# Optimization experiments

Measured on AMD Instinct MI355X. Metric: run time of the kernel, lower is better.

## Reference

```python
import jax, jax.numpy as jnp
import numpy as np

EPS = 1e-5

def batchnorm2d(x, gamma, beta):
    # training-mode BN over (N, T, V) per channel; x: [N, C, T, V]
    mean = jnp.mean(x, axis=(0, 2, 3), keepdims=True)
    var = jnp.var(x, axis=(0, 2, 3), keepdims=True)
    xhat = (x - mean) * jax.lax.rsqrt(var + EPS)
    return xhat * gamma[None, :, None, None] + beta[None, :, None, None]

def temporal_shift(x, theta, stride):
    # learnable per-channel temporal shift with linear interpolation, zero pad
    # x: [N, C, T, V], theta: [C]
    N, C, T, V = x.shape
    T_out = T // stride
    t = jnp.arange(T_out, dtype=theta.dtype)
    pos = t[None, :] * stride + theta[:, None]          # [C, T_out]
    i0 = jnp.floor(pos).astype(jnp.int32)
    frac = (pos - i0.astype(theta.dtype))[None, :, :, None]  # [1,C,T_out,1]
    cidx = jnp.arange(C)[:, None]                        # [C, 1]

    def gather(idx):
        valid = (idx >= 0) & (idx < T)
        g = x[:, cidx, jnp.clip(idx, 0, T - 1), :]       # [N, C, T_out, V]
        return jnp.where(valid[None, :, :, None], g, 0.0)

    return gather(i0) * (1.0 - frac) + gather(i0 + 1) * frac

def setup_inputs() -> dict:
    key = jax.random.key(0)
    k = jax.random.split(key, 6)
    N, Cin, Cout, T, V = 64, 256, 256, 64, 25
    x = jax.random.normal(k[0], (N, Cin, T, V), dtype=jnp.float32)
    # kaiming normal fan_out for 1x1 conv: std = sqrt(2 / (Cout*1*1))
    conv_w = jax.random.normal(k[1], (Cout, Cin), dtype=jnp.float32) * np.float32(np.sqrt(2.0 / Cout))
    conv_b = jnp.zeros((Cout,), dtype=jnp.float32)
    bn1_g = jnp.ones((Cin,), dtype=jnp.float32)
    bn1_b = jnp.zeros((Cin,), dtype=jnp.float32)
    bn2_g = jnp.ones((Cin,), dtype=jnp.float32)   # bn_init(bn2, 1)
    bn2_b = jnp.zeros((Cin,), dtype=jnp.float32)
    theta_in = jax.random.uniform(k[2], (Cin,), jnp.float32, -1.0, 1.0)
    theta_out = jax.random.uniform(k[3], (Cout,), jnp.float32, -1.0, 1.0)
    return {"x": x, "conv_w": conv_w, "conv_b": conv_b,
            "bn1_g": bn1_g, "bn1_b": bn1_b, "bn2_g": bn2_g, "bn2_b": bn2_b,
            "theta_in": theta_in, "theta_out": theta_out}

def reference(x, conv_w, conv_b, bn1_g, bn1_b, bn2_g, bn2_b, theta_in, theta_out):
    stride = 1
    h = batchnorm2d(x, bn1_g, bn1_b)
    h = temporal_shift(h, theta_in, 1)
    h = jnp.einsum('nctv,oc->notv', h, conv_w) + conv_b[None, :, None, None]
    h = jax.nn.relu(h)
    h = temporal_shift(h, theta_out, stride)
    h = batchnorm2d(h, bn2_g, bn2_b)
    return h
```

## Files before the change

### kernel.cpp

```cpp
#include <hip/hip_runtime.h>


#define EPSV 1e-5f
constexpr int Nn = 64, Cc = 256, Tt = 64, Vv = 25;
constexpr int TV = Tt * Vv;
constexpr int CTV = Cc * TV;
constexpr float Minv = 1.0f / (Nn * TV);

typedef short short8 __attribute__((ext_vector_type(8)));
typedef float floatx4 __attribute__((ext_vector_type(4)));

__device__ __forceinline__ unsigned short f2bf(float f) {
    unsigned int u = __builtin_bit_cast(unsigned int, f);
    u += 0x7FFFu + ((u >> 16) & 1u);
    return (unsigned short)(u >> 16);
}
__device__ __forceinline__ float bf2f(unsigned short h) {
    unsigned int u = ((unsigned int)h) << 16;
    return __builtin_bit_cast(float, u);
}
__device__ __forceinline__ void gload_lds16(const void* g, void* l) {
    __builtin_amdgcn_global_load_lds((const __attribute__((address_space(1))) void*)g,
                                     (__attribute__((address_space(3))) void*)l, 16, 0, 0);
}

__global__ __launch_bounds__(256) void k_stats_shift(const float* __restrict__ x,
                                                     const float* __restrict__ theta,
                                                     float* __restrict__ sacc,
                                                     float* __restrict__ qacc,
                                                     unsigned short* __restrict__ ht) {
    int c0 = blockIdx.x * 64;
    int E0 = blockIdx.y * 200;
    int n  = blockIdx.z;
    int tid = threadIdx.x;
    __shared__ __attribute__((aligned(16))) float xt[256][68];
    __shared__ int   pd[64];
    __shared__ float pf[64];
    if (tid < 64) {
        float th = theta[c0 + tid];
        float fd = floorf(th);
        pd[tid] = (int)fd;
        pf[tid] = th - fd;
    }
    int lo = E0 - 28; if (lo < 0) lo = 0;
    int hi = E0 + 228; if (hi > 1600) hi = 1600;
    int ldsoff = lo - (E0 - 28);
    int nf4 = (hi - lo) >> 2;
    {
        int ci = tid >> 2, li = tid & 3;
        const float4* xrow = (const float4*)(x + (size_t)n * CTV + (size_t)(c0 + ci) * TV + lo);
        for (int i = li; i < nf4; i += 4) {
            float4 v = xrow[i];
            int r = ldsoff + i * 4;
            xt[r][ci] = v.x; xt[r + 1][ci] = v.y; xt[r + 2][ci] = v.z; xt[r + 3][ci] = v.w;
        }
    }
    __syncthreads();
    {
        int ci = tid >> 2, li = tid & 3;
        float s = 0.f, q = 0.f;
        for (int r = 28 + li; r < 228; r += 4) {
            float v = xt[r][ci];
            s += v; q += v * v;
        }
        s += __shfl_down(s, 2); q += __shfl_down(q, 2);
        s += __shfl_down(s, 1); q += __shfl_down(q, 1);
        if (li == 0) { atomicAdd(&sacc[c0 + ci], s); atomicAdd(&qacc[c0 + ci], q); }
    }
    int cseg = tid & 7, er = tid >> 3;
    int cb = cseg * 8;
    for (int it = 0; it < 7; ++it) {
        int tv_l = er + it * 32;
        if (tv_l >= 200) break;
        int e = E0 + tv_l;
        int t = e / 25;
        const float* rA = &xt[tv_l + 3][cb];
        const float* rB = &xt[tv_l + 28][cb];
        const float* rC = &xt[tv_l + 53][cb];
        float4 a0 = *(const float4*)rA, a1 = *(const float4*)(rA + 4);
        float4 b0 = *(const float4*)rB, b1 = *(const float4*)(rB + 4);
        float4 g0 = *(const float4*)rC, g1 = *(const float4*)(rC + 4);
        float A8[8] = {a0.x, a0.y, a0.z, a0.w, a1.x, a1.y, a1.z, a1.w};
        float B8[8] = {b0.x, b0.y, b0.z, b0.w, b1.x, b1.y, b1.z, b1.w};
        float C8[8] = {g0.x, g0.y, g0.z, g0.w, g1.x, g1.y, g1.z, g1.w};
        unsigned int w4[4];
#pragma unroll
        for (int k = 0; k < 8; ++k) {
            int c = cb + k;
            int d = pd[c]; float f = pf[c];
            int i0 = t + d;
            float x0 = (d < 0) ? A8[k] : B8[k];
            float x1 = (d < 0) ? B8[k] : C8[k];
            float v0 = ((unsigned)i0 < 64u) ? x0 : 0.f;
            float v1 = ((unsigned)(i0 + 1) < 64u) ? x1 : 0.f;
            unsigned short hb = f2bf(v0 + f * (v1 - v0));
            if (k & 1) w4[k >> 1] |= ((unsigned int)hb) << 16;
            else       w4[k >> 1] = hb;
        }
        uint4 st = { w4[0], w4[1], w4[2], w4[3] };
        *(uint4*)(ht + (size_t)(n * 1600 + e) * 256 + c0 + cb) = st;
    }
}

__global__ __launch_bounds__(256) void k_params(const float* __restrict__ w,
                                                const float* __restrict__ bias,
                                                const float* __restrict__ sacc,
                                                const float* __restrict__ qacc,
                                                const float* __restrict__ g,
                                                const float* __restrict__ b,
                                                const float* __restrict__ theta,
                                                unsigned short* __restrict__ wb,
                                                float* __restrict__ b2all,
                                                float* __restrict__ s0v,
                                                float* __restrict__ s63v) {
    int o = blockIdx.x, c = threadIdx.x;
    float mean = sacc[c] * Minv;
    float var  = qacc[c] * Minv - mean * mean;
    float sc = g[c] * rsqrtf(var + EPSV);
    float tc = b[c] - mean * sc;
    float th = theta[c];
    float fd = floorf(th);
    int d = (int)fd;
    float f = th - fd;
    float wv = w[o * 256 + c];
    wb[o * 256 + c] = f2bf(wv * sc);
    float wtc = wv * tc;
    float r0  = (d < 0) ? wtc * (1.f - f) : 0.f;
    float r63 = (d == 0) ? wtc * f : 0.f;
    for (int off = 32; off; off >>= 1) {
        wtc += __shfl_down(wtc, off);
        r0  += __shfl_down(r0, off);
        r63 += __shfl_down(r63, off);
    }
    __shared__ float aux[3][4];
    if ((c & 63) == 0) { int wv_i = c >> 6; aux[0][wv_i] = wtc; aux[1][wv_i] = r0; aux[2][wv_i] = r63; }
    __syncthreads();
    if (c == 0) {
        float sw  = aux[0][0] + aux[0][1] + aux[0][2] + aux[0][3];
        float s0  = aux[1][0] + aux[1][1] + aux[1][2] + aux[1][3];
        float s63 = aux[2][0] + aux[2][1] + aux[2][2] + aux[2][3];
        b2all[o] = bias[o] + sw;
        s0v[o] = s0;
        s63v[o] = s63;
    }
}

__global__ __launch_bounds__(256, 2) void k_gemm(const unsigned short* __restrict__ ht,
                                                 const unsigned short* __restrict__ wb,
                                                 const float* __restrict__ b2all,
                                                 const float* __restrict__ s0v,
                                                 const float* __restrict__ s63v,
                                                 unsigned short* __restrict__ y) {
    int j0 = blockIdx.x * 128;
    int tid = threadIdx.x;
    int w = tid >> 6, lane = tid & 63;
    int quad = lane >> 4, l16 = lane & 15;
    __shared__ __attribute__((aligned(16))) unsigned short smem[256 * 136];
    unsigned short* A = smem;
    unsigned short* B = smem + 256 * 32;
    floatx4 acc[4][8] = {};
    int srowA = w * 64 + (lane >> 2);
    int srowB = w * 32 + (lane >> 2);
    int skc = (lane & 3) * 8;
    const unsigned short* wp = wb + (size_t)srowA * 256 + skc;
    const unsigned short* hp = ht + (size_t)(j0 + srowB) * 256 + skc;
    for (int k0 = 0; k0 < 256; k0 += 32) {
        __syncthreads();
#pragma unroll
        for (int a = 0; a < 4; ++a)
            gload_lds16(wp + (size_t)a * 16 * 256 + k0, A + (w * 64 + a * 16) * 32);
#pragma unroll
        for (int a = 0; a < 2; ++a)
            gload_lds16(hp + (size_t)a * 16 * 256 + k0, B + (w * 32 + a * 16) * 32);
        __syncthreads();
        short8 af[4], bf[8];
#pragma unroll
        for (int m = 0; m < 4; ++m)
            af[m] = *(const short8*)&A[(w * 64 + m * 16 + l16) * 32 + quad * 8];
#pragma unroll
        for (int jt = 0; jt < 8; ++jt)
            bf[jt] = *(const short8*)&B[(jt * 16 + l16) * 32 + quad * 8];
#pragma unroll
        for (int m = 0; m < 4; ++m)
#pragma unroll
            for (int jt = 0; jt < 8; ++jt)
                acc[m][jt] = __builtin_amdgcn_mfma_f32_16x16x32_bf16(af[m], bf[jt], acc[m][jt], 0, 0, 0);
    }
    __syncthreads();
    unsigned short* Cl = smem;
#pragma unroll
    for (int m = 0; m < 4; ++m) {
        int ob = w * 64 + m * 16 + quad * 4;
#pragma unroll
        for (int r = 0; r < 4; ++r) {
            int o = ob + r;
            float bb = b2all[o], e0 = s0v[o], e63 = s63v[o];
#pragma unroll
            for (int jt = 0; jt < 8; ++jt) {
                int jj = j0 + jt * 16;
                int nn = jj / 1600;
                int tvb = jj - nn * 1600 + l16;
                float bia = bb - (tvb < 25 ? e0 : 0.f) - (tvb >= 1575 ? e63 : 0.f);
                float v = acc[m][jt][r] + bia;
                v = v > 0.f ? v : 0.f;
                Cl[o * 136 + jt * 16 + l16] = f2bf(v);
            }
        }
    }
    __syncthreads();
    int li = tid & 15, orow = tid >> 4;
#pragma unroll
    for (int pass = 0; pass < 16; ++pass) {
        int o = orow + pass * 16;
        uint4 vv = *(const uint4*)&Cl[o * 136 + li * 8];
        int j = j0 + li * 8;
        int nn = j / 1600;
        int tv = j - nn * 1600;
        *(uint4*)(y + (size_t)nn * CTV + (size_t)o * TV + tv) = vv;
    }
}

__global__ __launch_bounds__(256) void k_bn2_stats(const unsigned short* __restrict__ y,
                                                   const float* __restrict__ theta,
                                                   float* __restrict__ sacc,
                                                   float* __restrict__ qacc) {
    int o = blockIdx.y, ng = blockIdx.x, tid = threadIdx.x;
    __shared__ __attribute__((aligned(16))) unsigned short row[1600];
    float th = theta[o];
    float fd = floorf(th);
    int d = (int)fd;
    float f = th - fd;
    float s = 0.f, q = 0.f;
    for (int n = ng * 8; n < ng * 8 + 8; ++n) {
        const uint4* yp = (const uint4*)(y + (size_t)n * CTV + (size_t)o * TV);
        __syncthreads();
        if (tid < 200) ((uint4*)row)[tid] = yp[tid];
        __syncthreads();
        for (int e = tid; e < 1600; e += 256) {
            int t = e / 25, v = e - t * 25;
            int i0 = t + d, i1 = i0 + 1;
            float a0 = ((unsigned)i0 < 64u) ? bf2f(row[i0 * 25 + v]) : 0.f;
            float a1 = ((unsigned)i1 < 64u) ? bf2f(row[i1 * 25 + v]) : 0.f;
            float z = (1.f - f) * a0 + f * a1;
            s += z; q += z * z;
        }
    }
    for (int off = 32; off; off >>= 1) { s += __shfl_down(s, off); q += __shfl_down(q, off); }
    if ((tid & 63) == 0) { atomicAdd(&sacc[o], s); atomicAdd(&qacc[o], q); }
}

__global__ __launch_bounds__(256) void k_bn2_apply(const unsigned short* __restrict__ y,
                                                   const float* __restrict__ theta,
                                                   const float* __restrict__ sacc,
                                                   const float* __restrict__ qacc,
                                                   const float* __restrict__ g,
                                                   const float* __restrict__ b,
                                                   float* __restrict__ out) {
    int o = blockIdx.y, n = blockIdx.x, tid = threadIdx.x;
    __shared__ __attribute__((aligned(16))) unsigned short row[1600];
    float th = theta[o];
    float fd = floorf(th);
    int d = (int)fd;
    float f = th - fd;
    float mean = sacc[o] * Minv;
    float var = qacc[o] * Minv - mean * mean;
    float sc = g[o] * rsqrtf(var + EPSV);
    float tc = b[o] - mean * sc;
    const uint4* yp = (const uint4*)(y + (size_t)n * CTV + (size_t)o * TV);
    if (tid < 200) ((uint4*)row)[tid] = yp[tid];
    __syncthreads();
    float4* op = (float4*)(out + (size_t)n * CTV + (size_t)o * TV);
    for (int i = tid; i < 400; i += 256) {
        float4 r;
        int e = i * 4;
#pragma unroll
        for (int k = 0; k < 4; ++k) {
            int ee = e + k;
            int t = ee / 25, v = ee - t * 25;
            int i0 = t + d, i1 = i0 + 1;
            float a0 = ((unsigned)i0 < 64u) ? bf2f(row[i0 * 25 + v]) : 0.f;
            float a1 = ((unsigned)i1 < 64u) ? bf2f(row[i1 * 25 + v]) : 0.f;
            ((float*)&r)[k] = ((1.f - f) * a0 + f * a1) * sc + tc;
        }
        op[i] = r;
    }
}

extern "C" void kernel_launch(void* const* d_in, const int* in_sizes, int n_in,
                              void* d_out, int out_size, void* d_ws, size_t ws_size,
                              hipStream_t stream) {
    const float* x      = (const float*)d_in[0];
    const float* conv_w = (const float*)d_in[1];
    const float* conv_b = (const float*)d_in[2];
    const float* bn1_g  = (const float*)d_in[3];
    const float* bn1_b  = (const float*)d_in[4];
    const float* bn2_g  = (const float*)d_in[5];
    const float* bn2_b  = (const float*)d_in[6];
    const float* th_in  = (const float*)d_in[7];
    const float* th_out = (const float*)d_in[8];
    float* out = (float*)d_out;

    char* ws = (char*)d_ws;
    unsigned short* ht = (unsigned short*)ws;
    unsigned short* yy = (unsigned short*)(ws + 52428800);
    unsigned short* wb = (unsigned short*)(ws + 104857600);
    float* sacc1 = (float*)(ws + 104988672);
    float* qacc1 = sacc1 + 256;
    float* sacc2 = qacc1 + 256;
    float* qacc2 = sacc2 + 256;
    float* b2all = qacc2 + 256;
    float* s0v   = b2all + 256;
    float* s63v  = s0v + 256;

    hipMemsetAsync((void*)sacc1, 0, 4 * 256 * sizeof(float), stream);
    hipLaunchKernelGGL(k_stats_shift, dim3(4, 8, 64), dim3(256), 0, stream,
                       x, th_in, sacc1, qacc1, ht);
    hipLaunchKernelGGL(k_params, dim3(256), dim3(256), 0, stream,
                       conv_w, conv_b, sacc1, qacc1, bn1_g, bn1_b, th_in,
                       wb, b2all, s0v, s63v);
    hipLaunchKernelGGL(k_gemm, dim3(800), dim3(256), 0, stream,
                       ht, wb, b2all, s0v, s63v, yy);
    hipLaunchKernelGGL(k_bn2_stats, dim3(8, 256), dim3(256), 0, stream, yy, th_out, sacc2, qacc2);
    hipLaunchKernelGGL(k_bn2_apply, dim3(64, 256), dim3(256), 0, stream,
                       yy, th_out, sacc2, qacc2, bn2_g, bn2_b, out);
}
```

Measured before the change: 315.7 us.

## Derive BN2 stats algebraically from raw moments; bf16 LDS staging in shift kernel

```diff
diff --git a/kernel.cpp b/kernel.cpp
--- a/kernel.cpp
+++ b/kernel.cpp
@@ -18,6 +18,16 @@
 __device__ __forceinline__ float bf2f(unsigned short h) {
     unsigned int u = ((unsigned int)h) << 16;
     return __builtin_bit_cast(float, u);
+}
+__device__ __forceinline__ float bflo(unsigned int w) {
+    return __builtin_bit_cast(float, w << 16);
+}
+__device__ __forceinline__ float bfhi(unsigned int w) {
+    return __builtin_bit_cast(float, w & 0xFFFF0000u);
+}
+__device__ __forceinline__ void unp8v(uint4 u, float* o) {
+    o[0] = bflo(u.x); o[1] = bfhi(u.x); o[2] = bflo(u.y); o[3] = bfhi(u.y);
+    o[4] = bflo(u.z); o[5] = bfhi(u.z); o[6] = bflo(u.w); o[7] = bfhi(u.w);
 }
 __device__ __forceinline__ void gload_lds16(const void* g, void* l) {
     __builtin_amdgcn_global_load_lds((const __attribute__((address_space(1))) void*)g,
@@ -33,7 +43,7 @@
     int E0 = blockIdx.y * 200;
     int n  = blockIdx.z;
     int tid = threadIdx.x;
-    __shared__ __attribute__((aligned(16))) float xt[256][68];
+    __shared__ __attribute__((aligned(16))) unsigned short xt[256][68];
     __shared__ int   pd[64];
     __shared__ float pf[64];
     if (tid < 64) {
@@ -47,52 +57,67 @@
     int ldsoff = lo - (E0 - 28);
     int nf4 = (hi - lo) >> 2;
     {
-        int ci = tid >> 2, li = tid & 3;
-        const float4* xrow = (const float4*)(x + (size_t)n * CTV + (size_t)(c0 + ci) * TV + lo);
-        for (int i = li; i < nf4; i += 4) {
-            float4 v = xrow[i];
+        int cp = tid >> 3, li = tid & 7;
+        int ca = 2 * cp;
+        const float4* xr0 = (const float4*)(x + (size_t)n * CTV + (size_t)(c0 + ca) * TV + lo);
+        const float4* xr1 = (const float4*)(x + (size_t)n * CTV + (size_t)(c0 + ca + 1) * TV + lo);
+        float s0 = 0.f, q0 = 0.f, s1 = 0.f, q1 = 0.f;
+        for (int i = li; i < nf4; i += 8) {
+            float4 v0 = xr0[i], v1 = xr1[i];
             int r = ldsoff + i * 4;
-            xt[r][ci] = v.x; xt[r + 1][ci] = v.y; xt[r + 2][ci] = v.z; xt[r + 3][ci] = v.w;
+#pragma unroll
+            for (int k = 0; k < 4; ++k) {
+                float a = ((const float*)&v0)[k];
+                float b = ((const float*)&v1)[k];
+                bool in = (unsigned)(r + k - 28) < 200u;
+                if (in) { s0 += a; q0 += a * a; s1 += b; q1 += b * b; }
+                unsigned int pk = (unsigned int)f2bf(a) | (((unsigned int)f2bf(b)) << 16);
+                *(unsigned int*)&xt[r + k][ca] = pk;
+            }
+        }
+        for (int off = 4; off; off >>= 1) {
+            s0 += __shfl_down(s0, off); q0 += __shfl_down(q0, off);
+            s1 += __shfl_down(s1, off); q1 += __shfl_down(q1, off);
+        }
+        if (li == 0) {
+            atomicAdd(&sacc[c0 + ca], s0);     atomicAdd(&qacc[c0 + ca], q0);
+            atomicAdd(&sacc[c0 + ca + 1], s1); atomicAdd(&qacc[c0 + ca + 1], q1);
         }
     }
     __syncthreads();
-    {
-        int ci = tid >> 2, li = tid & 3;
-        float s = 0.f, q = 0.f;
-        for (int r = 28 + li; r < 228; r += 4) {
-            float v = xt[r][ci];
-            s += v; q += v * v;
-        }
-        s += __shfl_down(s, 2); q += __shfl_down(q, 2);
-        s += __shfl_down(s, 1); q += __shfl_down(q, 1);
-        if (li == 0) { atomicAdd(&sacc[c0 + ci], s); atomicAdd(&qacc[c0 + ci], q); }
-    }
     int cseg = tid & 7, er = tid >> 3;
     int cb = cseg * 8;
+    int dk[8]; float fk[8];
+#pragma unroll
+    for (int k = 0; k < 8; ++k) { dk[k] = pd[cb + k]; fk[k] = pf[cb + k]; }
     for (int it = 0; it < 7; ++it) {
         int tv_l = er + it * 32;
         if (tv_l >= 200) break;
         int e = E0 + tv_l;
-        int t = e / 25;
-        const float* rA = &xt[tv_l + 3][cb];
-        const float* rB = &xt[tv_l + 28][cb];
-        const float* rC = &xt[tv_l + 53][cb];
-        float4 a0 = *(const float4*)rA, a1 = *(const float4*)(rA + 4);
-        float4 b0 = *(const float4*)rB, b1 = *(const float4*)(rB + 4);
-        float4 g0 = *(const float4*)rC, g1 = *(const float4*)(rC + 4);
-        float A8[8] = {a0.x, a0.y, a0.z, a0.w, a1.x, a1.y, a1.z, a1.w};
-        float B8[8] = {b0.x, b0.y, b0.z, b0.w, b1.x, b1.y, b1.z, b1.w};
-        float C8[8] = {g0.x, g0.y, g0.z, g0.w, g1.x, g1.y, g1.z, g1.w};
+        float A8[8], B8[8], C8[8];
+        {
+            const unsigned short* rA = &xt[tv_l + 3][cb];
+            const unsigned short* rB = &xt[tv_l + 28][cb];
+            const unsigned short* rC = &xt[tv_l + 53][cb];
+            uint2 a0 = *(const uint2*)rA, a1 = *(const uint2*)(rA + 4);
+            uint2 b0 = *(const uint2*)rB, b1 = *(const uint2*)(rB + 4);
+            uint2 g0 = *(const uint2*)rC, g1 = *(const uint2*)(rC + 4);
+            A8[0]=bflo(a0.x); A8[1]=bfhi(a0.x); A8[2]=bflo(a0.y); A8[3]=bfhi(a0.y);
+            A8[4]=bflo(a1.x); A8[5]=bfhi(a1.x); A8[6]=bflo(a1.y); A8[7]=bfhi(a1.y);
+            B8[0]=bflo(b0.x); B8[1]=bfhi(b0.x); B8[2]=bflo(b0.y); B8[3]=bfhi(b0.y);
+            B8[4]=bflo(b1.x); B8[5]=bfhi(b1.x); B8[6]=bflo(b1.y); B8[7]=bfhi(b1.y);
+            C8[0]=bflo(g0.x); C8[1]=bfhi(g0.x); C8[2]=bflo(g0.y); C8[3]=bfhi(g0.y);
+            C8[4]=bflo(g1.x); C8[5]=bfhi(g1.x); C8[6]=bflo(g1.y); C8[7]=bfhi(g1.y);
+        }
         unsigned int w4[4];
 #pragma unroll
         for (int k = 0; k < 8; ++k) {
-            int c = cb + k;
-            int d = pd[c]; float f = pf[c];
-            int i0 = t + d;
+            int d = dk[k]; float f = fk[k];
             float x0 = (d < 0) ? A8[k] : B8[k];
             float x1 = (d < 0) ? B8[k] : C8[k];
-            float v0 = ((unsigned)i0 < 64u) ? x0 : 0.f;
-            float v1 = ((unsigned)(i0 + 1) < 64u) ? x1 : 0.f;
+            int e0 = e + 25 * d;
+            float v0 = ((unsigned)e0 < 1600u) ? x0 : 0.f;
+            float v1 = ((unsigned)(e0 + 25) < 1600u) ? x1 : 0.f;
             unsigned short hb = f2bf(v0 + f * (v1 - v0));
             if (k & 1) w4[k >> 1] |= ((unsigned int)hb) << 16;
             else       w4[k >> 1] = hb;
@@ -133,15 +158,12 @@
         r63 += __shfl_down(r63, off);
     }
     __shared__ float aux[3][4];
-    if ((c & 63) == 0) { int wv_i = c >> 6; aux[0][wv_i] = wtc; aux[1][wv_i] = r0; aux[2][wv_i] = r63; }
+    if ((c & 63) == 0) { int wi = c >> 6; aux[0][wi] = wtc; aux[1][wi] = r0; aux[2][wi] = r63; }
     __syncthreads();
     if (c == 0) {
-        float sw  = aux[0][0] + aux[0][1] + aux[0][2] + aux[0][3];
-        float s0  = aux[1][0] + aux[1][1] + aux[1][2] + aux[1][3];
-        float s63 = aux[2][0] + aux[2][1] + aux[2][2] + aux[2][3];
-        b2all[o] = bias[o] + sw;
-        s0v[o] = s0;
-        s63v[o] = s63;
+        b2all[o] = bias[o] + aux[0][0] + aux[0][1] + aux[0][2] + aux[0][3];
+        s0v[o]  = aux[1][0] + aux[1][1] + aux[1][2] + aux[1][3];
+        s63v[o] = aux[2][0] + aux[2][1] + aux[2][2] + aux[2][3];
     }
 }
 
@@ -221,69 +243,111 @@
 }
 
 __global__ __launch_bounds__(256) void k_bn2_stats(const unsigned short* __restrict__ y,
+                                                   float* __restrict__ acc7) {
+    int o = blockIdx.y, ng = blockIdx.x, tid = threadIdx.x;
+    float S = 0.f, Q = 0.f, P = 0.f, Y0 = 0.f, Q0 = 0.f, Y63 = 0.f, Q63 = 0.f;
+    if (tid < 200) {
+        int e = tid * 8;
+        int eB = e + 24; if (eB > 1592) eB = 1592;
+        int eC = e + 32; if (eC > 1592) eC = 1592;
+        const unsigned short* base0 = y + (size_t)(ng * 8) * CTV + (size_t)o * TV;
+        for (int nn = 0; nn < 8; ++nn) {
+            const unsigned short* row = base0 + (size_t)nn * CTV;
+            float a[8], b[8], c[8];
+            unp8v(*(const uint4*)(row + e), a);
+            unp8v(*(const uint4*)(row + eB), b);
+            unp8v(*(const uint4*)(row + eC), c);
+#pragma unroll
+            for (int k = 0; k < 8; ++k) {
+                float v = a[k];
+                S += v; Q += v * v;
+                float vn = (k < 7) ? b[k + 1] : c[0];
+                if (e + k < 1575) P += v * vn;
+            }
+            if (e < 32) {
+#pragma unroll
+                for (int k = 0; k < 8; ++k)
+                    if (e + k < 25) { Y0 += a[k]; Q0 += a[k] * a[k]; }
+            }
+            if (e >= 1568) {
+#pragma unroll
+                for (int k = 0; k < 8; ++k)
+                    if (e + k >= 1575) { Y63 += a[k]; Q63 += a[k] * a[k]; }
+            }
+        }
+    }
+    for (int off = 32; off; off >>= 1) {
+        S += __shfl_down(S, off); Q += __shfl_down(Q, off); P += __shfl_down(P, off);
+        Y0 += __shfl_down(Y0, off); Q0 += __shfl_down(Q0, off);
+        Y63 += __shfl_down(Y63, off); Q63 += __shfl_down(Q63, off);
+    }
+    if ((tid & 63) == 0) {
+        atomicAdd(&acc7[o], S);           atomicAdd(&acc7[256 + o], Q);
+        atomicAdd(&acc7[512 + o], P);     atomicAdd(&acc7[768 + o], Y0);
+        atomicAdd(&acc7[1024 + o], Q0);   atomicAdd(&acc7[1280 + o], Y63);
+        atomicAdd(&acc7[1536 + o], Q63);
+    }
+}
+
+__global__ __launch_bounds__(256) void k_bn2_apply(const unsigned short* __restrict__ y,
                                                    const float* __restrict__ theta,
-                                                   float* __restrict__ sacc,
-                                                   float* __restrict__ qacc) {
-    int o = blockIdx.y, ng = blockIdx.x, tid = threadIdx.x;
-    __shared__ __attribute__((aligned(16))) unsigned short row[1600];
+                                                   const float* __restrict__ acc7,
+                                                   const float* __restrict__ g,
+                                                   const float* __restrict__ b,
+                                                   float* __restrict__ out) {
+    int o = blockIdx.y, n = blockIdx.x, tid = threadIdx.x;
     float th = theta[o];
     float fd = floorf(th);
     int d = (int)fd;
     float f = th - fd;
-    float s = 0.f, q = 0.f;
-    for (int n = ng * 8; n < ng * 8 + 8; ++n) {
-        const uint4* yp = (const uint4*)(y + (size_t)n * CTV + (size_t)o * TV);
-        __syncthreads();
-        if (tid < 200) ((uint4*)row)[tid] = yp[tid];
-        __syncthreads();
-        for (int e = tid; e < 1600; e += 256) {
-            int t = e / 25, v = e - t * 25;
-            int i0 = t + d, i1 = i0 + 1;
-            float a0 = ((unsigned)i0 < 64u) ? bf2f(row[i0 * 25 + v]) : 0.f;
-            float a1 = ((unsigned)i1 < 64u) ? bf2f(row[i1 * 25 + v]) : 0.f;
-            float z = (1.f - f) * a0 + f * a1;
-            s += z; q += z * z;
-        }
-    }
-    for (int off = 32; off; off >>= 1) { s += __shfl_down(s, off); q += __shfl_down(q, off); }
-    if ((tid & 63) == 0) { atomicAdd(&sacc[o], s); atomicAdd(&qacc[o], q); }
-}
-
-__global__ __launch_bounds__(256) void k_bn2_apply(const unsigned short* __restrict__ y,
-                                                   const float* __restrict__ theta,
-                                                   const float* __restrict__ sacc,
-                                                   const float* __restrict__ qacc,
-                                                   const float* __restrict__ g,
-                                                   const float* __restrict__ b,
-                                                   float* __restrict__ out) {
-    int o = blockIdx.y, n = blockIdx.x, tid = threadIdx.x;
-    __shared__ __attribute__((aligned(16))) unsigned short row[1600];
-    float th = theta[o];
-    float fd = floorf(th);
-    int d = (int)fd;
-    float f = th - fd;
-    float mean = sacc[o] * Minv;
-    float var = qacc[o] * Minv - mean * mean;
+    float S = acc7[o], Q = acc7[256 + o], P = acc7[512 + o];
+    float Y0 = acc7[768 + o], Q0 = acc7[1024 + o], Y63 = acc7[1280 + o], Q63 = acc7[1536 + o];
+    float omf = 1.f - f;
+    float sz, qz;
+    if (d < 0) { sz = S - omf * Y63; qz = omf * omf * (Q - Q63) + f * f * Q + 2.f * f * omf * P; }
+    else       { sz = S - f * Y0;    qz = omf * omf * Q + f * f * (Q - Q0) + 2.f * f * omf * P; }
+    float mean = sz * Minv;
+    float var = qz * Minv - mean * mean;
     float sc = g[o] * rsqrtf(var + EPSV);
     float tc = b[o] - mean * sc;
-    const uint4* yp = (const uint4*)(y + (size_t)n * CTV + (size_t)o * TV);
-    if (tid < 200) ((uint4*)row)[tid] = yp[tid];
-    __syncthreads();
-    float4* op = (float4*)(out + (size_t)n * CTV + (size_t)o * TV);
-    for (int i = tid; i < 400; i += 256) {
-        float4 r;
-        int e = i * 4;
-#pragma unroll
-        for (int k = 0; k < 4; ++k) {
-            int ee = e + k;
-            int t = ee / 25, v = ee - t * 25;
-            int i0 = t + d, i1 = i0 + 1;
-            float a0 = ((unsigned)i0 < 64u) ? bf2f(row[i0 * 25 + v]) : 0.f;
-            float a1 = ((unsigned)i1 < 64u) ? bf2f(row[i1 * 25 + v]) : 0.f;
-            ((float*)&r)[k] = ((1.f - f) * a0 + f * a1) * sc + tc;
-        }
-        op[i] = r;
-    }
+    if (tid >= 200) return;
+    int e = tid * 8;
+    const unsigned short* row = y + (size_t)n * CTV + (size_t)o * TV;
+    float a0[8], a1[8];
+    if (d < 0) {
+        int eA = e - 32; if (eA < 0) eA = 0;
+        int eB = e - 24; if (eB < 0) eB = 0;
+        float A[8], B[8], M[8];
+        unp8v(*(const uint4*)(row + eA), A);
+        unp8v(*(const uint4*)(row + eB), B);
+        unp8v(*(const uint4*)(row + e), M);
+        a0[0] = (e >= 25) ? A[7] : 0.f;
+#pragma unroll
+        for (int k = 1; k < 8; ++k) a0[k] = (e + k >= 25) ? B[k - 1] : 0.f;
+#pragma unroll
+        for (int k = 0; k < 8; ++k) a1[k] = M[k];
+    } else {
+        int eB = e + 24; if (eB > 1592) eB = 1592;
+        int eC = e + 32; if (eC > 1592) eC = 1592;
+        float M[8], B[8], C[8];
+        unp8v(*(const uint4*)(row + e), M);
+        unp8v(*(const uint4*)(row + eB), B);
+        unp8v(*(const uint4*)(row + eC), C);
+#pragma unroll
+        for (int k = 0; k < 8; ++k) a0[k] = M[k];
+#pragma unroll
+        for (int k = 0; k < 7; ++k) a1[k] = (e + k < 1575) ? B[k + 1] : 0.f;
+        a1[7] = (e + 7 < 1575) ? C[0] : 0.f;
+    }
+    float4 r0, r1;
+#pragma unroll
+    for (int k = 0; k < 4; ++k) {
+        ((float*)&r0)[k] = (omf * a0[k] + f * a1[k]) * sc + tc;
+        ((float*)&r1)[k] = (omf * a0[k + 4] + f * a1[k + 4]) * sc + tc;
+    }
+    float* op = out + (size_t)n * CTV + (size_t)o * TV + e;
+    *(float4*)op = r0;
+    *(float4*)(op + 4) = r1;
 }
 
 extern "C" void kernel_launch(void* const* d_in, const int* in_sizes, int n_in,
@@ -306,13 +370,12 @@
     unsigned short* wb = (unsigned short*)(ws + 104857600);
     float* sacc1 = (float*)(ws + 104988672);
     float* qacc1 = sacc1 + 256;
-    float* sacc2 = qacc1 + 256;
-    float* qacc2 = sacc2 + 256;
-    float* b2all = qacc2 + 256;
+    float* acc7  = qacc1 + 256;
+    float* b2all = acc7 + 7 * 256;
     float* s0v   = b2all + 256;
     float* s63v  = s0v + 256;
 
-    hipMemsetAsync((void*)sacc1, 0, 4 * 256 * sizeof(float), stream);
+    hipMemsetAsync((void*)sacc1, 0, 9 * 256 * sizeof(float), stream);
     hipLaunchKernelGGL(k_stats_shift, dim3(4, 8, 64), dim3(256), 0, stream,
                        x, th_in, sacc1, qacc1, ht);
     hipLaunchKernelGGL(k_params, dim3(256), dim3(256), 0, stream,
@@ -320,7 +383,7 @@
                        wb, b2all, s0v, s63v);
     hipLaunchKernelGGL(k_gemm, dim3(800), dim3(256), 0, stream,
                        ht, wb, b2all, s0v, s63v, yy);
-    hipLaunchKernelGGL(k_bn2_stats, dim3(8, 256), dim3(256), 0, stream, yy, th_out, sacc2, qacc2);
+    hipLaunchKernelGGL(k_bn2_stats, dim3(8, 256), dim3(256), 0, stream, yy, acc7);
     hipLaunchKernelGGL(k_bn2_apply, dim3(64, 256), dim3(256), 0, stream,
-                       yy, th_out, sacc2, qacc2, bn2_g, bn2_b, out);
-}
+                       yy, th_out, acc7, bn2_g, bn2_b, out);
+}
```

Result: slower. 342.5 us (+8.5%).
